# Performance work log

Hardware: AMD Instinct MI355X
Metric: run time of the kernel (lower is better)

Reference implementation:

```python
import jax, jax.numpy as jnp
import numpy as np

DEPTH, HEADS, DIM_HEAD, DIM = 4, 8, 64, 512
B, N = 4, 512
SCALE = DIM_HEAD ** -0.5  # attention scale
EPS = 1e-5


def _ln(r, g, b):
    # naive real-valued LayerNorm over last dim
    m = jnp.mean(r, -1, keepdims=True)
    v = jnp.mean((r - m) ** 2, -1, keepdims=True)
    return (r - m) / jnp.sqrt(v + EPS) * g + b


def _cln(z, gr, br, gi, bi):
    # 'layer_norm_naive': LN applied separately to real and imag parts
    return jax.lax.complex(_ln(jnp.real(z), gr, br), _ln(jnp.imag(z), gi, bi))


def _csoftmax(z):
    # softmax on magnitude, phase preserved (Eq. 36, arXiv:1802.08026)
    p = jax.nn.softmax(jnp.abs(z), axis=-1)
    ph = jnp.angle(z)
    return jax.lax.complex(p * jnp.cos(ph), p * jnp.sin(ph))


def _crelu(z):
    return jax.lax.complex(jax.nn.relu(jnp.real(z)), jax.nn.relu(jnp.imag(z)))


def setup_inputs():
    key = jax.random.key(0)
    ks = jax.random.split(key, 8)
    s = np.float32(1.0 / np.sqrt(DIM))
    return dict(
        x_real=jax.random.normal(ks[0], (B, N, DIM), jnp.float32),
        x_imag=jax.random.normal(ks[1], (B, N, DIM), jnp.float32),
        ln1_g_r=jnp.ones((DEPTH, DIM), jnp.float32),
        ln1_b_r=jnp.zeros((DEPTH, DIM), jnp.float32),
        ln1_g_i=jnp.ones((DEPTH, DIM), jnp.float32),
        ln1_b_i=jnp.zeros((DEPTH, DIM), jnp.float32),
        ln2_g_r=jnp.ones((DEPTH, DIM), jnp.float32),
        ln2_b_r=jnp.zeros((DEPTH, DIM), jnp.float32),
        ln2_g_i=jnp.ones((DEPTH, DIM), jnp.float32),
        ln2_b_i=jnp.zeros((DEPTH, DIM), jnp.float32),
        qkv_w_r=jax.random.normal(ks[2], (DEPTH, DIM, DIM), jnp.float32) * s,
        qkv_w_i=jax.random.normal(ks[3], (DEPTH, DIM, DIM), jnp.float32) * s,
        out_w_r=jax.random.normal(ks[4], (DEPTH, DIM, DIM), jnp.float32) * s,
        out_w_i=jax.random.normal(ks[5], (DEPTH, DIM, DIM), jnp.float32) * s,
        out_b_r=jnp.zeros((DEPTH, DIM), jnp.float32),
        out_b_i=jnp.zeros((DEPTH, DIM), jnp.float32),
        ff_w_r=jax.random.normal(ks[6], (DEPTH, DIM, DIM), jnp.float32) * s,
        ff_w_i=jax.random.normal(ks[7], (DEPTH, DIM, DIM), jnp.float32) * s,
        step_size=jnp.full((DEPTH,), 0.1, jnp.float32),
        lambd=jnp.full((DEPTH,), 0.1, jnp.float32),
    )


def reference(x_real, x_imag,
              ln1_g_r, ln1_b_r, ln1_g_i, ln1_b_i,
              ln2_g_r, ln2_b_r, ln2_g_i, ln2_b_i,
              qkv_w_r, qkv_w_i, out_w_r, out_w_i, out_b_r, out_b_i,
              ff_w_r, ff_w_i, step_size, lambd):
    x = jax.lax.complex(x_real, x_imag)  # [B, N, DIM] complex64
    for l in range(DEPTH):
        Wqkv = jax.lax.complex(qkv_w_r[l], qkv_w_i[l])  # [inner, dim]
        Wout = jax.lax.complex(out_w_r[l], out_w_i[l])  # [dim, inner]
        bout = jax.lax.complex(out_b_r[l], out_b_i[l])
        Wff = jax.lax.complex(ff_w_r[l], ff_w_i[l])     # [dim, dim]
        # --- PreNorm + Attention (single shared QKV projection) + residual
        xn = _cln(x, ln1_g_r[l], ln1_b_r[l], ln1_g_i[l], ln1_b_i[l])
        w = jnp.einsum('bnd,ed->bne', xn, Wqkv)                 # complex linear, no bias
        w = w.reshape(B, N, HEADS, DIM_HEAD).transpose(0, 2, 1, 3)  # b h n d
        dots = jnp.einsum('bhnd,bhmd->bhnm', w, jnp.conj(w)) * SCALE
        attn = _csoftmax(dots)
        out = jnp.einsum('bhnm,bhmd->bhnd', attn, w)
        out = out.transpose(0, 2, 1, 3).reshape(B, N, HEADS * DIM_HEAD)
        out = jnp.einsum('bne,de->bnd', out, Wout) + bout
        x = out + x
        # --- PreNorm + ISTA-style FeedForward (CReLU); no outer residual
        xn = _cln(x, ln2_g_r[l], ln2_b_r[l], ln2_g_i[l], ln2_b_i[l])
        ss = jax.nn.softplus(step_size[l])
        lm = jax.nn.softplus(lambd[l])
        x1 = jnp.einsum('bnd,ed->bne', xn, Wff)
        x = _crelu(xn + ss * x1 - ss * lm)
    # stack real/imag so the output is a plain float tensor [2, B, N, DIM]
    return jnp.stack([jnp.real(x), jnp.imag(x)], axis=0)
```

## Files before the change

kernel.cpp:

```cpp
#include <hip/hip_runtime.h>
#include <math.h>

#define DEPTHL 4
#define HEADS 8
#define DH 64
#define DIM 512
#define BATCH 4
#define SEQ 512
#define ROWS (BATCH*SEQ)
#define SCALE 0.125f
#define LNEPS 1e-5f

typedef __attribute__((ext_vector_type(8))) short bfrag;
typedef __attribute__((ext_vector_type(4))) float ffrag;
#define MFMA(a,b,c) __builtin_amdgcn_mfma_f32_16x16x32_bf16(a, b, c, 0, 0, 0)

__device__ __forceinline__ unsigned short f2bf(float f) {
    unsigned int u = __float_as_uint(f);
    u += 0x7fffu + ((u >> 16) & 1u);
    return (unsigned short)(u >> 16);
}
__device__ __forceinline__ float bf2f(unsigned short b) {
    return __uint_as_float(((unsigned int)b) << 16);
}

__global__ __launch_bounds__(256) void convw(
    const float* __restrict__ s0, const float* __restrict__ s1,
    const float* __restrict__ s2, const float* __restrict__ s3,
    const float* __restrict__ s4, const float* __restrict__ s5,
    unsigned short* __restrict__ dst)
{
    int gid = blockIdx.x * 256 + threadIdx.x;
    int idx = gid * 4;
    int seg = idx >> 18;
    int off = idx & 262143;
    const float* s = seg == 0 ? s0 : seg == 1 ? s1 : seg == 2 ? s2 :
                     seg == 3 ? s3 : seg == 4 ? s4 : s5;
    float4 v = *(const float4*)(s + off);
    unsigned long long p = (unsigned long long)f2bf(v.x)
        | ((unsigned long long)f2bf(v.y) << 16)
        | ((unsigned long long)f2bf(v.z) << 32)
        | ((unsigned long long)f2bf(v.w) << 48);
    *(unsigned long long*)(dst + idx) = p;
}

__device__ __forceinline__ void blk_sum4(float& a, float& b, float& c, float& d) {
    __shared__ float s[16];
    #pragma unroll
    for (int o = 32; o; o >>= 1) {
        a += __shfl_xor(a, o); b += __shfl_xor(b, o);
        c += __shfl_xor(c, o); d += __shfl_xor(d, o);
    }
    int w = threadIdx.x >> 6;
    if ((threadIdx.x & 63) == 0) { s[w*4+0]=a; s[w*4+1]=b; s[w*4+2]=c; s[w*4+3]=d; }
    __syncthreads();
    a = s[0]+s[4]+s[8]+s[12];
    b = s[1]+s[5]+s[9]+s[13];
    c = s[2]+s[6]+s[10]+s[14];
    d = s[3]+s[7]+s[11]+s[15];
    __syncthreads();
}

__global__ __launch_bounds__(256) void ln_kernel(
    const float* __restrict__ xr, const float* __restrict__ xi,
    const float* __restrict__ gr, const float* __restrict__ br,
    const float* __restrict__ gi, const float* __restrict__ bi,
    unsigned short* __restrict__ outr, unsigned short* __restrict__ outi)
{
    int row = blockIdx.x, t = threadIdx.x;
    float2 vr = ((const float2*)(xr + (size_t)row*DIM))[t];
    float2 vi = ((const float2*)(xi + (size_t)row*DIM))[t];
    float sr = vr.x+vr.y, qr = vr.x*vr.x+vr.y*vr.y;
    float si = vi.x+vi.y, qi = vi.x*vi.x+vi.y*vi.y;
    blk_sum4(sr, qr, si, qi);
    float mr = sr*(1.f/DIM), mi_ = si*(1.f/DIM);
    float rr = 1.f/sqrtf(qr*(1.f/DIM)-mr*mr+LNEPS);
    float ri = 1.f/sqrtf(qi*(1.f/DIM)-mi_*mi_+LNEPS);
    float2 g2r = ((const float2*)gr)[t], b2r = ((const float2*)br)[t];
    float2 g2i = ((const float2*)gi)[t], b2i = ((const float2*)bi)[t];
    float o0 = (vr.x-mr)*rr*g2r.x + b2r.x;
    float o1 = (vr.y-mr)*rr*g2r.y + b2r.y;
    float o2 = (vi.x-mi_)*ri*g2i.x + b2i.x;
    float o3 = (vi.y-mi_)*ri*g2i.y + b2i.y;
    unsigned int pr = (unsigned int)f2bf(o0) | ((unsigned int)f2bf(o1) << 16);
    unsigned int pi = (unsigned int)f2bf(o2) | ((unsigned int)f2bf(o3) << 16);
    ((unsigned int*)(outr + (size_t)row*DIM))[t] = pr;
    ((unsigned int*)(outi + (size_t)row*DIM))[t] = pi;
}

template<int MODE>
__global__ __launch_bounds__(256, 4) void cgemm_mfma(
    const unsigned short* __restrict__ Ar, const unsigned short* __restrict__ Ai,
    const unsigned short* __restrict__ Wr, const unsigned short* __restrict__ Wi,
    unsigned short* __restrict__ Obr, unsigned short* __restrict__ Obi,
    float* __restrict__ Ofr, float* __restrict__ Ofi,
    const float* __restrict__ biasR, const float* __restrict__ biasI,
    const float* __restrict__ stepp, const float* __restrict__ lamb, int layer)
{
    int tid = threadIdx.x;
    int lane = tid & 63;
    int w = tid >> 6, wr = w >> 1, wc = w & 1;
    int lrow = lane & 15, lg = lane >> 4;
    int bm = blockIdx.x, bn = blockIdx.y;

    const unsigned short* pAr = Ar + (size_t)(bm*32 + wr*16 + lrow)*DIM + lg*8;
    const unsigned short* pAi = Ai + (size_t)(bm*32 + wr*16 + lrow)*DIM + lg*8;
    const unsigned short* pBr[2]; const unsigned short* pBi[2];
    #pragma unroll
    for (int nt = 0; nt < 2; ++nt) {
        int brow = bn*64 + wc*32 + nt*16 + lrow;
        pBr[nt] = Wr + (size_t)brow*DIM + lg*8;
        pBi[nt] = Wi + (size_t)brow*DIM + lg*8;
    }
    ffrag acc1[2], acc2[2], acci[2];
    #pragma unroll
    for (int nt = 0; nt < 2; ++nt) {
        acc1[nt] = (ffrag){0.f,0.f,0.f,0.f};
        acc2[nt] = (ffrag){0.f,0.f,0.f,0.f};
        acci[nt] = (ffrag){0.f,0.f,0.f,0.f};
    }

    bfrag a_r = *(const bfrag*)(pAr);
    bfrag a_i = *(const bfrag*)(pAi);
    bfrag b_r0 = *(const bfrag*)(pBr[0]), b_r1 = *(const bfrag*)(pBr[1]);
    bfrag b_i0 = *(const bfrag*)(pBi[0]), b_i1 = *(const bfrag*)(pBi[1]);

    #pragma unroll 2
    for (int k0 = 0; k0 < DIM - 32; k0 += 32) {
        bfrag na_r = *(const bfrag*)(pAr + k0 + 32);
        bfrag na_i = *(const bfrag*)(pAi + k0 + 32);
        bfrag nb_r0 = *(const bfrag*)(pBr[0] + k0 + 32);
        bfrag nb_r1 = *(const bfrag*)(pBr[1] + k0 + 32);
        bfrag nb_i0 = *(const bfrag*)(pBi[0] + k0 + 32);
        bfrag nb_i1 = *(const bfrag*)(pBi[1] + k0 + 32);
        acc1[0] = MFMA(a_r, b_r0, acc1[0]);
        acc2[0] = MFMA(a_i, b_i0, acc2[0]);
        acci[0] = MFMA(a_r, b_i0, acci[0]);
        acci[0] = MFMA(a_i, b_r0, acci[0]);
        acc1[1] = MFMA(a_r, b_r1, acc1[1]);
        acc2[1] = MFMA(a_i, b_i1, acc2[1]);
        acci[1] = MFMA(a_r, b_i1, acci[1]);
        acci[1] = MFMA(a_i, b_r1, acci[1]);
        a_r = na_r; a_i = na_i;
        b_r0 = nb_r0; b_r1 = nb_r1; b_i0 = nb_i0; b_i1 = nb_i1;
    }
    acc1[0] = MFMA(a_r, b_r0, acc1[0]);
    acc2[0] = MFMA(a_i, b_i0, acc2[0]);
    acci[0] = MFMA(a_r, b_i0, acci[0]);
    acci[0] = MFMA(a_i, b_r0, acci[0]);
    acc1[1] = MFMA(a_r, b_r1, acc1[1]);
    acc2[1] = MFMA(a_i, b_i1, acc2[1]);
    acci[1] = MFMA(a_r, b_i1, acci[1]);
    acci[1] = MFMA(a_i, b_r1, acci[1]);

    float ss = 0.f, sl = 0.f;
    if (MODE == 2) { ss = log1pf(expf(stepp[layer])); sl = ss * log1pf(expf(lamb[layer])); }

    #pragma unroll
    for (int nt = 0; nt < 2; ++nt) {
        int E = bn*64 + wc*32 + nt*16 + lrow;
        #pragma unroll
        for (int r = 0; r < 4; ++r) {
            int R = bm*32 + wr*16 + lg*4 + r;
            float re = acc1[nt][r] - acc2[nt][r];
            float im = acci[nt][r];
            if (MODE == 0) {
                int b = R >> 9, n = R & (SEQ-1);
                int h = E >> 6, d = E & 63;
                size_t off = (((size_t)(b*HEADS + h)*SEQ + n) << 6) + d;
                Obr[off] = f2bf(re);
                Obi[off] = f2bf(im);
            } else if (MODE == 1) {
                size_t off = (size_t)R*DIM + E;
                Ofr[off] = re + biasR[E] + Ofr[off];
                Ofi[off] = im + biasI[E] + Ofi[off];
            } else {
                size_t off = (size_t)R*DIM + E;
                float xnr_ = bf2f(Ar[off]), xni_ = bf2f(Ai[off]);
                Ofr[off] = fmaxf(xnr_ + ss*re - sl, 0.f);
                Ofi[off] = fmaxf(xni_ + ss*im, 0.f);
            }
        }
    }
}

#define SVI(w_, ri, d, m) ((((w_)*2 + (ri))*64 + (d))*40 + (m))
#define SPI(w_, ri, q, m) (20480 + (((w_)*2 + (ri))*16 + (q))*40 + (m))

__global__ __launch_bounds__(256, 3) void attn_mfma(
    const unsigned short* __restrict__ whr, const unsigned short* __restrict__ whi,
    unsigned short* __restrict__ aor, unsigned short* __restrict__ aoi)
{
    __shared__ __align__(16) unsigned short pool[25856];
    float* sMS = (float*)(pool + 25600);
    float* sAccR = (float*)pool;
    float* sAccI = sAccR + 64*16;

    int tid = threadIdx.x, lane = tid & 63, w = tid >> 6;
    int lrow = lane & 15, lg = lane >> 4;
    int bh = blockIdx.x, qt = blockIdx.y;
    const unsigned short* baseR = whr + ((size_t)bh << 15);
    const unsigned short* baseI = whi + ((size_t)bh << 15);
    int q0 = qt*16;

    bfrag qfr[2], qfi[2];
    #pragma unroll
    for (int ks = 0; ks < 2; ++ks) {
        qfr[ks] = *(const bfrag*)(baseR + ((size_t)(q0 + lrow) << 6) + ks*32 + lg*8);
        qfi[ks] = *(const bfrag*)(baseI + ((size_t)(q0 + lrow) << 6) + ks*32 + lg*8);
    }
    float M = -1e30f, S = 0.f;
    ffrag o1[4], o2[4], o3[4];
    #pragma unroll
    for (int dt = 0; dt < 4; ++dt) {
        o1[dt] = (ffrag){0.f,0.f,0.f,0.f};
        o2[dt] = (ffrag){0.f,0.f,0.f,0.f};
        o3[dt] = (ffrag){0.f,0.f,0.f,0.f};
    }
    const int sm = lane & 31;
    const int sdb = ((lane >> 5) & 1) * 8;

    #pragma unroll 1
    for (int rd = 0; rd < 4; ++rd) {
        int m0 = rd*128 + w*32;
        #pragma unroll
        for (int it = 0; it < 4; ++it) {
            int d0 = sdb + it*16;
            bfrag vr = *(const bfrag*)(baseR + ((size_t)(m0 + sm) << 6) + d0);
            bfrag vi = *(const bfrag*)(baseI + ((size_t)(m0 + sm) << 6) + d0);
            #pragma unroll
            for (int j = 0; j < 8; ++j) {
                pool[SVI(w, 0, d0 + j, sm)] = (unsigned short)vr[j];
                pool[SVI(w, 1, d0 + j, sm)] = (unsigned short)vi[j];
            }
        }
        ffrag zr[2], zp[2], zm_[2];
        #pragma unroll
        for (int t = 0; t < 2; ++t) {
            zr[t] = (ffrag){0.f,0.f,0.f,0.f};
            zp[t] = (ffrag){0.f,0.f,0.f,0.f};
            zm_[t] = (ffrag){0.f,0.f,0.f,0.f};
        }
        #pragma unroll
        for (int t = 0; t < 2; ++t)
        #pragma unroll
        for (int ks = 0; ks < 2; ++ks) {
            bfrag kr = *(const bfrag*)(baseR + ((size_t)(m0 + t*16 + lrow) << 6) + ks*32 + lg*8);
            bfrag ki = *(const bfrag*)(baseI + ((size_t)(m0 + t*16 + lrow) << 6) + ks*32 + lg*8);
            zr[t]  = MFMA(kr, qfr[ks], zr[t]);
            zr[t]  = MFMA(ki, qfi[ks], zr[t]);
            zp[t]  = MFMA(kr, qfi[ks], zp[t]);
            zm_[t] = MFMA(ki, qfr[ks], zm_[t]);
        }
        float av[2][4], rv[2][4], iv[2][4];
        float pmax = -1e30f;
        #pragma unroll
        for (int t = 0; t < 2; ++t)
        #pragma unroll
        for (int r = 0; r < 4; ++r) {
            float zrv = zr[t][r] * SCALE;
            float ziv = (zp[t][r] - zm_[t][r]) * SCALE;
            float a = sqrtf(zrv*zrv + ziv*ziv);
            av[t][r] = a; rv[t][r] = zrv; iv[t][r] = ziv;
            pmax = fmaxf(pmax, a);
        }
        pmax = fmaxf(pmax, __shfl_xor(pmax, 16));
        pmax = fmaxf(pmax, __shfl_xor(pmax, 32));
        float Mnew = fmaxf(M, pmax);
        float f = expf(M - Mnew);
        M = Mnew;
        S *= f;
        #pragma unroll
        for (int dt = 0; dt < 4; ++dt) { o1[dt] *= f; o2[dt] *= f; o3[dt] *= f; }
        float ssum = 0.f;
        #pragma unroll
        for (int t = 0; t < 2; ++t) {
            float ur[4], ui[4];
            #pragma unroll
            for (int r = 0; r < 4; ++r) {
                float a = av[t][r];
                float ee = expf(a - M);
                ssum += ee;
                float inva = a > 0.f ? ee / a : 0.f;
                ur[r] = a > 0.f ? inva * rv[t][r] : ee;
                ui[r] = inva * iv[t][r];
            }
            uint2 wpr, wpi;
            wpr.x = (unsigned int)f2bf(ur[0]) | ((unsigned int)f2bf(ur[1]) << 16);
            wpr.y = (unsigned int)f2bf(ur[2]) | ((unsigned int)f2bf(ur[3]) << 16);
            wpi.x = (unsigned int)f2bf(ui[0]) | ((unsigned int)f2bf(ui[1]) << 16);
            wpi.y = (unsigned int)f2bf(ui[2]) | ((unsigned int)f2bf(ui[3]) << 16);
            *(uint2*)&pool[SPI(w, 0, lrow, t*16 + lg*4)] = wpr;
            *(uint2*)&pool[SPI(w, 1, lrow, t*16 + lg*4)] = wpi;
        }
        ssum += __shfl_xor(ssum, 16);
        ssum += __shfl_xor(ssum, 32);
        S += ssum;
        bfrag pr = *(const bfrag*)&pool[SPI(w, 0, lrow, lg*8)];
        bfrag pi = *(const bfrag*)&pool[SPI(w, 1, lrow, lg*8)];
        #pragma unroll
        for (int dt = 0; dt < 4; ++dt) {
            bfrag vr = *(const bfrag*)&pool[SVI(w, 0, dt*16 + lrow, lg*8)];
            bfrag vi = *(const bfrag*)&pool[SVI(w, 1, dt*16 + lrow, lg*8)];
            o1[dt] = MFMA(vr, pr, o1[dt]);
            o2[dt] = MFMA(vi, pi, o2[dt]);
            o3[dt] = MFMA(vr, pi, o3[dt]);
            o3[dt] = MFMA(vi, pr, o3[dt]);
        }
    }

    if (lg == 0) { sMS[(w*2 + 0)*16 + lrow] = M; sMS[(w*2 + 1)*16 + lrow] = S; }
    __syncthreads();
    float Mf = -1e30f;
    #pragma unroll
    for (int w2 = 0; w2 < 4; ++w2) Mf = fmaxf(Mf, sMS[(w2*2 + 0)*16 + lrow]);
    float Sf = 0.f;
    #pragma unroll
    for (int w2 = 0; w2 < 4; ++w2)
        Sf += sMS[(w2*2 + 1)*16 + lrow] * expf(sMS[(w2*2 + 0)*16 + lrow] - Mf);
    float fac = expf(M - Mf) / Sf;

    #pragma unroll 1
    for (int ww = 0; ww < 4; ++ww) {
        if (w == ww) {
            #pragma unroll
            for (int dt = 0; dt < 4; ++dt)
            #pragma unroll
            for (int r = 0; r < 4; ++r) {
                int d = dt*16 + lg*4 + r;
                float vR = (o1[dt][r] - o2[dt][r]) * fac;
                float vI = o3[dt][r] * fac;
                if (ww == 0) { sAccR[d*16 + lrow] = vR; sAccI[d*16 + lrow] = vI; }
                else         { sAccR[d*16 + lrow] += vR; sAccI[d*16 + lrow] += vI; }
            }
        }
        __syncthreads();
    }
    {
        int q = tid >> 4, d0 = (tid & 15) * 4;
        int b = bh >> 3, h = bh & 7;
        float r0 = sAccR[(d0+0)*16 + q], r1 = sAccR[(d0+1)*16 + q];
        float r2 = sAccR[(d0+2)*16 + q], r3 = sAccR[(d0+3)*16 + q];
        float i0 = sAccI[(d0+0)*16 + q], i1 = sAccI[(d0+1)*16 + q];
        float i2 = sAccI[(d0+2)*16 + q], i3 = sAccI[(d0+3)*16 + q];
        uint2 pr, pi;
        pr.x = (unsigned int)f2bf(r0) | ((unsigned int)f2bf(r1) << 16);
        pr.y = (unsigned int)f2bf(r2) | ((unsigned int)f2bf(r3) << 16);
        pi.x = (unsigned int)f2bf(i0) | ((unsigned int)f2bf(i1) << 16);
        pi.y = (unsigned int)f2bf(i2) | ((unsigned int)f2bf(i3) << 16);
        size_t off = (((size_t)(bh >> 3)*SEQ + qt*16 + q) << 9) + (bh & 7)*64 + d0;
        *(uint2*)(aor + off) = pr;
        *(uint2*)(aoi + off) = pi;
    }
}

extern "C" void kernel_launch(void* const* d_in, const int* in_sizes, int n_in,
                              void* d_out, int out_size, void* d_ws, size_t ws_size,
                              hipStream_t stream)
{
    const float* x_real  = (const float*)d_in[0];
    const float* x_imag  = (const float*)d_in[1];
    const float* ln1_g_r = (const float*)d_in[2];
    const float* ln1_b_r = (const float*)d_in[3];
    const float* ln1_g_i = (const float*)d_in[4];
    const float* ln1_b_i = (const float*)d_in[5];
    const float* ln2_g_r = (const float*)d_in[6];
    const float* ln2_b_r = (const float*)d_in[7];
    const float* ln2_g_i = (const float*)d_in[8];
    const float* ln2_b_i = (const float*)d_in[9];
    const float* qkv_w_r = (const float*)d_in[10];
    const float* qkv_w_i = (const float*)d_in[11];
    const float* out_w_r = (const float*)d_in[12];
    const float* out_w_i = (const float*)d_in[13];
    const float* out_b_r = (const float*)d_in[14];
    const float* out_b_i = (const float*)d_in[15];
    const float* ff_w_r  = (const float*)d_in[16];
    const float* ff_w_i  = (const float*)d_in[17];
    const float* stepp   = (const float*)d_in[18];
    const float* lamb    = (const float*)d_in[19];

    const size_t SZ = (size_t)ROWS * DIM;
    const size_t WSEG = (size_t)DIM * DIM;
    float* xr = (float*)d_ws;
    float* xi = xr + SZ;
    unsigned short* xnr = (unsigned short*)(xi + SZ);
    unsigned short* xni = xnr + SZ;
    unsigned short* whr = xni + SZ;
    unsigned short* whi = whr + SZ;
    unsigned short* aor = whi + SZ;
    unsigned short* aoi = aor + SZ;
    unsigned short* wb  = aoi + SZ;

    float* outR = (float*)d_out;
    float* outI = outR + SZ;

    hipMemcpyAsync(xr, x_real, SZ*sizeof(float), hipMemcpyDeviceToDevice, stream);
    hipMemcpyAsync(xi, x_imag, SZ*sizeof(float), hipMemcpyDeviceToDevice, stream);

    for (int l = 0; l < DEPTHL; ++l) {
        const size_t WO = (size_t)l * WSEG;
        convw<<<1536, 256, 0, stream>>>(qkv_w_r + WO, qkv_w_i + WO, out_w_r + WO,
                                        out_w_i + WO, ff_w_r + WO, ff_w_i + WO, wb);
        ln_kernel<<<ROWS, 256, 0, stream>>>(xr, xi,
            ln1_g_r + l*DIM, ln1_b_r + l*DIM, ln1_g_i + l*DIM, ln1_b_i + l*DIM, xnr, xni);
        cgemm_mfma<0><<<dim3(64, 8), 256, 0, stream>>>(xnr, xni, wb, wb + WSEG,
            whr, whi, nullptr, nullptr, nullptr, nullptr, nullptr, nullptr, l);
        attn_mfma<<<dim3(32, 32), 256, 0, stream>>>(whr, whi, aor, aoi);
        cgemm_mfma<1><<<dim3(64, 8), 256, 0, stream>>>(aor, aoi, wb + 2*WSEG, wb + 3*WSEG,
            nullptr, nullptr, xr, xi, out_b_r + l*DIM, out_b_i + l*DIM, nullptr, nullptr, l);
        ln_kernel<<<ROWS, 256, 0, stream>>>(xr, xi,
            ln2_g_r + l*DIM, ln2_b_r + l*DIM, ln2_g_i + l*DIM, ln2_b_i + l*DIM, xnr, xni);
        float* dstR = (l == DEPTHL-1) ? outR : xr;
        float* dstI = (l == DEPTHL-1) ? outI : xi;
        cgemm_mfma<2><<<dim3(64, 8), 256, 0, stream>>>(xnr, xni, wb + 4*WSEG, wb + 5*WSEG,
            nullptr, nullptr, dstR, dstI, nullptr, nullptr, stepp, lamb, l);
    }
}
```

Before: 657.8 us.

## Share K/V tiles across four query tiles in attention; deepen GEMM k-prefetch

The attention kernel now uses 512-thread blocks that each handle 64 queries. Two groups of four waves split the key range and stage shared K/V tiles in LDS, so each staged tile serves four query tiles instead of one. This cuts redundant global loads of the key/value data, at the cost of more barriers, fewer blocks (256 instead of 1024), and a two-way softmax merge. Separately, the complex GEMM prefetches 64 k-elements per iteration instead of 32 and relaxes launch bounds to 2 blocks per SIMD, trading occupancy for more loads in flight.

```diff
diff --git a/kernel.cpp b/kernel.cpp
--- a/kernel.cpp
+++ b/kernel.cpp
@@ -89,7 +89,7 @@
 }
 
 template<int MODE>
-__global__ __launch_bounds__(256, 4) void cgemm_mfma(
+__global__ __launch_bounds__(256, 2) void cgemm_mfma(
     const unsigned short* __restrict__ Ar, const unsigned short* __restrict__ Ai,
     const unsigned short* __restrict__ Wr, const unsigned short* __restrict__ Wi,
     unsigned short* __restrict__ Obr, unsigned short* __restrict__ Obi,
@@ -105,13 +105,11 @@
 
     const unsigned short* pAr = Ar + (size_t)(bm*32 + wr*16 + lrow)*DIM + lg*8;
     const unsigned short* pAi = Ai + (size_t)(bm*32 + wr*16 + lrow)*DIM + lg*8;
-    const unsigned short* pBr[2]; const unsigned short* pBi[2];
-    #pragma unroll
-    for (int nt = 0; nt < 2; ++nt) {
-        int brow = bn*64 + wc*32 + nt*16 + lrow;
-        pBr[nt] = Wr + (size_t)brow*DIM + lg*8;
-        pBi[nt] = Wi + (size_t)brow*DIM + lg*8;
-    }
+    const unsigned short* pBr0 = Wr + (size_t)(bn*64 + wc*32 + lrow)*DIM + lg*8;
+    const unsigned short* pBi0 = Wi + (size_t)(bn*64 + wc*32 + lrow)*DIM + lg*8;
+    const unsigned short* pBr1 = pBr0 + (size_t)16*DIM;
+    const unsigned short* pBi1 = pBi0 + (size_t)16*DIM;
+
     ffrag acc1[2], acc2[2], acci[2];
     #pragma unroll
     for (int nt = 0; nt < 2; ++nt) {
@@ -120,38 +118,43 @@
         acci[nt] = (ffrag){0.f,0.f,0.f,0.f};
     }
 
-    bfrag a_r = *(const bfrag*)(pAr);
-    bfrag a_i = *(const bfrag*)(pAi);
-    bfrag b_r0 = *(const bfrag*)(pBr[0]), b_r1 = *(const bfrag*)(pBr[1]);
-    bfrag b_i0 = *(const bfrag*)(pBi[0]), b_i1 = *(const bfrag*)(pBi[1]);
+    bfrag ar0  = *(const bfrag*)(pAr),       ar1  = *(const bfrag*)(pAr + 32);
+    bfrag ai0  = *(const bfrag*)(pAi),       ai1  = *(const bfrag*)(pAi + 32);
+    bfrag br00 = *(const bfrag*)(pBr0),      br01 = *(const bfrag*)(pBr0 + 32);
+    bfrag br10 = *(const bfrag*)(pBr1),      br11 = *(const bfrag*)(pBr1 + 32);
+    bfrag bi00 = *(const bfrag*)(pBi0),      bi01 = *(const bfrag*)(pBi0 + 32);
+    bfrag bi10 = *(const bfrag*)(pBi1),      bi11 = *(const bfrag*)(pBi1 + 32);
 
     #pragma unroll 2
-    for (int k0 = 0; k0 < DIM - 32; k0 += 32) {
-        bfrag na_r = *(const bfrag*)(pAr + k0 + 32);
-        bfrag na_i = *(const bfrag*)(pAi + k0 + 32);
-        bfrag nb_r0 = *(const bfrag*)(pBr[0] + k0 + 32);
-        bfrag nb_r1 = *(const bfrag*)(pBr[1] + k0 + 32);
-        bfrag nb_i0 = *(const bfrag*)(pBi[0] + k0 + 32);
-        bfrag nb_i1 = *(const bfrag*)(pBi[1] + k0 + 32);
-        acc1[0] = MFMA(a_r, b_r0, acc1[0]);
-        acc2[0] = MFMA(a_i, b_i0, acc2[0]);
-        acci[0] = MFMA(a_r, b_i0, acci[0]);
-        acci[0] = MFMA(a_i, b_r0, acci[0]);
-        acc1[1] = MFMA(a_r, b_r1, acc1[1]);
-        acc2[1] = MFMA(a_i, b_i1, acc2[1]);
-        acci[1] = MFMA(a_r, b_i1, acci[1]);
-        acci[1] = MFMA(a_i, b_r1, acci[1]);
-        a_r = na_r; a_i = na_i;
-        b_r0 = nb_r0; b_r1 = nb_r1; b_i0 = nb_i0; b_i1 = nb_i1;
-    }
-    acc1[0] = MFMA(a_r, b_r0, acc1[0]);
-    acc2[0] = MFMA(a_i, b_i0, acc2[0]);
-    acci[0] = MFMA(a_r, b_i0, acci[0]);
-    acci[0] = MFMA(a_i, b_r0, acci[0]);
-    acc1[1] = MFMA(a_r, b_r1, acc1[1]);
-    acc2[1] = MFMA(a_i, b_i1, acc2[1]);
-    acci[1] = MFMA(a_r, b_i1, acci[1]);
-    acci[1] = MFMA(a_i, b_r1, acci[1]);
+    for (int k0 = 0; k0 < DIM - 64; k0 += 64) {
+        bfrag nar0  = *(const bfrag*)(pAr  + k0 + 64), nar1  = *(const bfrag*)(pAr  + k0 + 96);
+        bfrag nai0  = *(const bfrag*)(pAi  + k0 + 64), nai1  = *(const bfrag*)(pAi  + k0 + 96);
+        bfrag nbr00 = *(const bfrag*)(pBr0 + k0 + 64), nbr01 = *(const bfrag*)(pBr0 + k0 + 96);
+        bfrag nbr10 = *(const bfrag*)(pBr1 + k0 + 64), nbr11 = *(const bfrag*)(pBr1 + k0 + 96);
+        bfrag nbi00 = *(const bfrag*)(pBi0 + k0 + 64), nbi01 = *(const bfrag*)(pBi0 + k0 + 96);
+        bfrag nbi10 = *(const bfrag*)(pBi1 + k0 + 64), nbi11 = *(const bfrag*)(pBi1 + k0 + 96);
+
+        acc1[0] = MFMA(ar0, br00, acc1[0]);  acc1[0] = MFMA(ar1, br01, acc1[0]);
+        acc2[0] = MFMA(ai0, bi00, acc2[0]);  acc2[0] = MFMA(ai1, bi01, acc2[0]);
+        acci[0] = MFMA(ar0, bi00, acci[0]);  acci[0] = MFMA(ai0, br00, acci[0]);
+        acci[0] = MFMA(ar1, bi01, acci[0]);  acci[0] = MFMA(ai1, br01, acci[0]);
+        acc1[1] = MFMA(ar0, br10, acc1[1]);  acc1[1] = MFMA(ar1, br11, acc1[1]);
+        acc2[1] = MFMA(ai0, bi10, acc2[1]);  acc2[1] = MFMA(ai1, bi11, acc2[1]);
+        acci[1] = MFMA(ar0, bi10, acci[1]);  acci[1] = MFMA(ai0, br10, acci[1]);
+        acci[1] = MFMA(ar1, bi11, acci[1]);  acci[1] = MFMA(ai1, br11, acci[1]);
+
+        ar0 = nar0; ar1 = nar1; ai0 = nai0; ai1 = nai1;
+        br00 = nbr00; br01 = nbr01; br10 = nbr10; br11 = nbr11;
+        bi00 = nbi00; bi01 = nbi01; bi10 = nbi10; bi11 = nbi11;
+    }
+    acc1[0] = MFMA(ar0, br00, acc1[0]);  acc1[0] = MFMA(ar1, br01, acc1[0]);
+    acc2[0] = MFMA(ai0, bi00, acc2[0]);  acc2[0] = MFMA(ai1, bi01, acc2[0]);
+    acci[0] = MFMA(ar0, bi00, acci[0]);  acci[0] = MFMA(ai0, br00, acci[0]);
+    acci[0] = MFMA(ar1, bi01, acci[0]);  acci[0] = MFMA(ai1, br01, acci[0]);
+    acc1[1] = MFMA(ar0, br10, acc1[1]);  acc1[1] = MFMA(ar1, br11, acc1[1]);
+    acc2[1] = MFMA(ai0, bi10, acc2[1]);  acc2[1] = MFMA(ai1, bi11, acc2[1]);
+    acci[1] = MFMA(ar0, bi10, acci[1]);  acci[1] = MFMA(ai0, br10, acci[1]);
+    acci[1] = MFMA(ar1, bi11, acci[1]);  acci[1] = MFMA(ai1, br11, acci[1]);
 
     float ss = 0.f, sl = 0.f;
     if (MODE == 2) { ss = log1pf(expf(stepp[layer])); sl = ss * log1pf(expf(lamb[layer])); }
@@ -184,24 +187,25 @@
     }
 }
 
-#define SVI(w_, ri, d, m) ((((w_)*2 + (ri))*64 + (d))*40 + (m))
-#define SPI(w_, ri, q, m) (20480 + (((w_)*2 + (ri))*16 + (q))*40 + (m))
-
-__global__ __launch_bounds__(256, 3) void attn_mfma(
+#define SVI(g_, ri, d, m) ((((g_)*2 + (ri))*64 + (d))*40 + (m))
+#define SPI(w_, ri, q, m) (10240 + (((w_)*2 + (ri))*16 + (q))*40 + (m))
+
+__global__ __launch_bounds__(512, 1) void attn_mfma(
     const unsigned short* __restrict__ whr, const unsigned short* __restrict__ whi,
     unsigned short* __restrict__ aor, unsigned short* __restrict__ aoi)
 {
-    __shared__ __align__(16) unsigned short pool[25856];
-    float* sMS = (float*)(pool + 25600);
+    __shared__ __align__(16) unsigned short pool[20992];
+    float* sMS  = (float*)(pool + 20480);
     float* sAccR = (float*)pool;
-    float* sAccI = sAccR + 64*16;
+    float* sAccI = sAccR + 4096;
 
     int tid = threadIdx.x, lane = tid & 63, w = tid >> 6;
+    int qw = w & 3, g = w >> 2;
     int lrow = lane & 15, lg = lane >> 4;
     int bh = blockIdx.x, qt = blockIdx.y;
     const unsigned short* baseR = whr + ((size_t)bh << 15);
     const unsigned short* baseI = whi + ((size_t)bh << 15);
-    int q0 = qt*16;
+    int q0 = qt*64 + qw*16;
 
     bfrag qfr[2], qfi[2];
     #pragma unroll
@@ -217,21 +221,20 @@
         o2[dt] = (ffrag){0.f,0.f,0.f,0.f};
         o3[dt] = (ffrag){0.f,0.f,0.f,0.f};
     }
-    const int sm = lane & 31;
-    const int sdb = ((lane >> 5) & 1) * 8;
+    int t8 = tid & 255;
+    int sm = t8 & 31, sdb = (t8 >> 5) * 8;
 
     #pragma unroll 1
-    for (int rd = 0; rd < 4; ++rd) {
-        int m0 = rd*128 + w*32;
-        #pragma unroll
-        for (int it = 0; it < 4; ++it) {
-            int d0 = sdb + it*16;
-            bfrag vr = *(const bfrag*)(baseR + ((size_t)(m0 + sm) << 6) + d0);
-            bfrag vi = *(const bfrag*)(baseI + ((size_t)(m0 + sm) << 6) + d0);
+    for (int it = 0; it < 8; ++it) {
+        int m0 = g*256 + it*32;
+        __syncthreads();
+        {
+            bfrag vr = *(const bfrag*)(baseR + ((size_t)(m0 + sm) << 6) + sdb);
+            bfrag vi = *(const bfrag*)(baseI + ((size_t)(m0 + sm) << 6) + sdb);
             #pragma unroll
             for (int j = 0; j < 8; ++j) {
-                pool[SVI(w, 0, d0 + j, sm)] = (unsigned short)vr[j];
-                pool[SVI(w, 1, d0 + j, sm)] = (unsigned short)vi[j];
+                pool[SVI(g, 0, sdb + j, sm)] = (unsigned short)vr[j];
+                pool[SVI(g, 1, sdb + j, sm)] = (unsigned short)vi[j];
             }
         }
         ffrag zr[2], zp[2], zm_[2];
@@ -296,12 +299,13 @@
         ssum += __shfl_xor(ssum, 16);
         ssum += __shfl_xor(ssum, 32);
         S += ssum;
+        __syncthreads();
         bfrag pr = *(const bfrag*)&pool[SPI(w, 0, lrow, lg*8)];
         bfrag pi = *(const bfrag*)&pool[SPI(w, 1, lrow, lg*8)];
         #pragma unroll
         for (int dt = 0; dt < 4; ++dt) {
-            bfrag vr = *(const bfrag*)&pool[SVI(w, 0, dt*16 + lrow, lg*8)];
-            bfrag vi = *(const bfrag*)&pool[SVI(w, 1, dt*16 + lrow, lg*8)];
+            bfrag vr = *(const bfrag*)&pool[SVI(g, 0, dt*16 + lrow, lg*8)];
+            bfrag vi = *(const bfrag*)&pool[SVI(g, 1, dt*16 + lrow, lg*8)];
             o1[dt] = MFMA(vr, pr, o1[dt]);
             o2[dt] = MFMA(vi, pi, o2[dt]);
             o3[dt] = MFMA(vr, pi, o3[dt]);
@@ -311,46 +315,51 @@
 
     if (lg == 0) { sMS[(w*2 + 0)*16 + lrow] = M; sMS[(w*2 + 1)*16 + lrow] = S; }
     __syncthreads();
-    float Mf = -1e30f;
-    #pragma unroll
-    for (int w2 = 0; w2 < 4; ++w2) Mf = fmaxf(Mf, sMS[(w2*2 + 0)*16 + lrow]);
-    float Sf = 0.f;
-    #pragma unroll
-    for (int w2 = 0; w2 < 4; ++w2)
-        Sf += sMS[(w2*2 + 1)*16 + lrow] * expf(sMS[(w2*2 + 0)*16 + lrow] - Mf);
+    int wp = w ^ 4;
+    float Mp = sMS[(wp*2 + 0)*16 + lrow], Sp = sMS[(wp*2 + 1)*16 + lrow];
+    float Mf = fmaxf(M, Mp);
+    float Sf = S*expf(M - Mf) + Sp*expf(Mp - Mf);
     float fac = expf(M - Mf) / Sf;
 
-    #pragma unroll 1
-    for (int ww = 0; ww < 4; ++ww) {
-        if (w == ww) {
-            #pragma unroll
-            for (int dt = 0; dt < 4; ++dt)
-            #pragma unroll
-            for (int r = 0; r < 4; ++r) {
-                int d = dt*16 + lg*4 + r;
-                float vR = (o1[dt][r] - o2[dt][r]) * fac;
-                float vI = o3[dt][r] * fac;
-                if (ww == 0) { sAccR[d*16 + lrow] = vR; sAccI[d*16 + lrow] = vI; }
-                else         { sAccR[d*16 + lrow] += vR; sAccI[d*16 + lrow] += vI; }
-            }
-        }
-        __syncthreads();
-    }
+    if (g == 1) {
+        #pragma unroll
+        for (int dt = 0; dt < 4; ++dt)
+        #pragma unroll
+        for (int r = 0; r < 4; ++r) {
+            int d = dt*16 + lg*4 + r;
+            sAccR[(qw*64 + d)*16 + lrow] = (o1[dt][r] - o2[dt][r]) * fac;
+            sAccI[(qw*64 + d)*16 + lrow] = o3[dt][r] * fac;
+        }
+    }
+    __syncthreads();
+    if (g == 0) {
+        #pragma unroll
+        for (int dt = 0; dt < 4; ++dt)
+        #pragma unroll
+        for (int r = 0; r < 4; ++r) {
+            int d = dt*16 + lg*4 + r;
+            sAccR[(qw*64 + d)*16 + lrow] += (o1[dt][r] - o2[dt][r]) * fac;
+            sAccI[(qw*64 + d)*16 + lrow] += o3[dt][r] * fac;
+        }
+    }
+    __syncthreads();
     {
-        int q = tid >> 4, d0 = (tid & 15) * 4;
+        int row = tid >> 3, d0 = (tid & 7) * 8;
+        int qb = row >> 4, qr = row & 15;
+        unsigned int pr[4], pi[4];
+        #pragma unroll
+        for (int jj = 0; jj < 4; ++jj) {
+            float r0 = sAccR[(qb*64 + d0 + 2*jj + 0)*16 + qr];
+            float r1 = sAccR[(qb*64 + d0 + 2*jj + 1)*16 + qr];
+            float i0 = sAccI[(qb*64 + d0 + 2*jj + 0)*16 + qr];
+            float i1 = sAccI[(qb*64 + d0 + 2*jj + 1)*16 + qr];
+            pr[jj] = (unsigned int)f2bf(r0) | ((unsigned int)f2bf(r1) << 16);
+            pi[jj] = (unsigned int)f2bf(i0) | ((unsigned int)f2bf(i1) << 16);
+        }
         int b = bh >> 3, h = bh & 7;
-        float r0 = sAccR[(d0+0)*16 + q], r1 = sAccR[(d0+1)*16 + q];
-        float r2 = sAccR[(d0+2)*16 + q], r3 = sAccR[(d0+3)*16 + q];
-        float i0 = sAccI[(d0+0)*16 + q], i1 = sAccI[(d0+1)*16 + q];
-        float i2 = sAccI[(d0+2)*16 + q], i3 = sAccI[(d0+3)*16 + q];
-        uint2 pr, pi;
-        pr.x = (unsigned int)f2bf(r0) | ((unsigned int)f2bf(r1) << 16);
-        pr.y = (unsigned int)f2bf(r2) | ((unsigned int)f2bf(r3) << 16);
-        pi.x = (unsigned int)f2bf(i0) | ((unsigned int)f2bf(i1) << 16);
-        pi.y = (unsigned int)f2bf(i2) | ((unsigned int)f2bf(i3) << 16);
-        size_t off = (((size_t)(bh >> 3)*SEQ + qt*16 + q) << 9) + (bh & 7)*64 + d0;
-        *(uint2*)(aor + off) = pr;
-        *(uint2*)(aoi + off) = pi;
+        size_t off = (((size_t)(b*SEQ + qt*64 + row)) << 9) + h*64 + d0;
+        *(uint4*)(aor + off) = make_uint4(pr[0], pr[1], pr[2], pr[3]);
+        *(uint4*)(aoi + off) = make_uint4(pi[0], pi[1], pi[2], pi[3]);
     }
 }
 
@@ -405,7 +414,7 @@
             ln1_g_r + l*DIM, ln1_b_r + l*DIM, ln1_g_i + l*DIM, ln1_b_i + l*DIM, xnr, xni);
         cgemm_mfma<0><<<dim3(64, 8), 256, 0, stream>>>(xnr, xni, wb, wb + WSEG,
             whr, whi, nullptr, nullptr, nullptr, nullptr, nullptr, nullptr, l);
-        attn_mfma<<<dim3(32, 32), 256, 0, stream>>>(whr, whi, aor, aoi);
+        attn_mfma<<<dim3(32, 8), 512, 0, stream>>>(whr, whi, aor, aoi);
         cgemm_mfma<1><<<dim3(64, 8), 256, 0, stream>>>(aor, aoi, wb + 2*WSEG, wb + 3*WSEG,
             nullptr, nullptr, xr, xi, out_b_r + l*DIM, out_b_i + l*DIM, nullptr, nullptr, l);
         ln_kernel<<<ROWS, 256, 0, stream>>>(xr, xi,
```

Measured after the change: 636.1 us. 3.3% less time.
